# Performance work log

Hardware: AMD Instinct MI355X
Metric: run time of the kernel (lower is better)

## Reference

```python
import jax, jax.numpy as jnp
import numpy as np

EPS = 1e-5
NEG_SLOPE = 0.2

def _bn(x, gamma, beta):
    # BatchNorm1d in training mode: stats over (batch, length) per channel. x: [B,C,N]
    m = jnp.mean(x, axis=(0, 2), keepdims=True)
    v = jnp.mean((x - m) ** 2, axis=(0, 2), keepdims=True)  # biased variance
    return (x - m) * jax.lax.rsqrt(v + EPS) * gamma[None, :, None] + beta[None, :, None]

def setup_inputs() -> dict:
    key = jax.random.key(0)
    ks = jax.random.split(key, 7)
    B, C, N, H = 32, 64, 2048, 128
    s = 1.0 / np.sqrt(C)
    return {
        "x": jax.random.normal(ks[0], (B, C, N), dtype=jnp.float32),
        "wq": jax.random.normal(ks[1], (C, C), dtype=jnp.float32) * s,
        "wk": jax.random.normal(ks[2], (C, C), dtype=jnp.float32) * s,
        "wv": jax.random.normal(ks[3], (C, C), dtype=jnp.float32) * s,
        "w_ff1": jax.random.normal(ks[4], (H, C), dtype=jnp.float32) * s,
        "w_ff2": jax.random.normal(ks[5], (C, H), dtype=jnp.float32) * (1.0 / np.sqrt(H)),
        "bn1_gamma": jnp.ones((C,), dtype=jnp.float32),
        "bn1_beta": jnp.zeros((C,), dtype=jnp.float32),
        "bn2_gamma": jnp.ones((C,), dtype=jnp.float32),
        "bn2_beta": jnp.zeros((C,), dtype=jnp.float32),
    }

def reference(x, wq, wk, wv, w_ff1, w_ff2, bn1_gamma, bn1_beta, bn2_gamma, bn2_beta):
    # x: [B, C, N]; 1x1 convs are per-point channel matmuls
    C = x.shape[1]
    q = jnp.einsum('oc,bcn->bno', wq, x)          # [B,N,C]
    k = jnp.einsum('oc,bcn->bon', wk, x)          # [B,C,N]
    v = jnp.einsum('oc,bcn->bno', wv, x)          # [B,N,C] (v^T)
    energy = jnp.einsum('bnc,bcm->bnm', q, k)     # [B,N,N]
    attention = jax.nn.softmax(energy / jnp.sqrt(jnp.float32(C)), axis=-1)
    x_r = jnp.einsum('bnm,bmc->bcn', attention, v)  # [B,C,N]
    h = _bn(x + x_r, bn1_gamma, bn1_beta)
    ff = jnp.einsum('hc,bcn->bhn', w_ff1, h)      # [B,H,N]
    ff = jnp.where(ff >= 0, ff, NEG_SLOPE * ff)   # LeakyReLU(0.2)
    ff = jnp.einsum('ch,bhn->bcn', w_ff2, ff)     # [B,C,N]
    return _bn(h + ff, bn2_gamma, bn2_beta)
```

## Files before the change

### kernel.cpp

```cpp
#include <hip/hip_runtime.h>

#define B_ 32
#define C_ 64
#define N_ 2048
#define H_ 128
#define MSHIFT 12.0f

typedef unsigned short u16;
typedef unsigned int u32;
typedef float f32x4 __attribute__((ext_vector_type(4)));
typedef float f32x16 __attribute__((ext_vector_type(16)));
typedef __bf16 bf16x8 __attribute__((ext_vector_type(8)));
typedef __bf16 bf16x4 __attribute__((ext_vector_type(4)));
typedef unsigned short u16x4 __attribute__((ext_vector_type(4)));
typedef unsigned int u32x4v __attribute__((ext_vector_type(4)));

#define MFMA(a, b, c) __builtin_amdgcn_mfma_f32_16x16x32_bf16(a, b, c, 0, 0, 0)
#define MFMA32(a, b, c) __builtin_amdgcn_mfma_f32_32x32x16_bf16(a, b, c, 0, 0, 0)
#define EXP2(x) __builtin_amdgcn_exp2f(x)
#define LOG2E 1.44269504088896f

__device__ __forceinline__ int swz(int row, int cb) { return row * 128 + (cb ^ ((row & 7) << 4)); }
__device__ __forceinline__ int swz256(int row, int cb) { return row * 256 + (cb ^ ((row & 7) << 4)); }

__device__ __forceinline__ float b2f(u16 v) {
    union { u32 u; float f; } x; x.u = ((u32)v) << 16; return x.f;
}

__device__ __forceinline__ u32 cvtpk(float lo, float hi) {
    u32 r;
    asm("v_cvt_pk_bf16_f32 %0, %1, %2" : "=v"(r) : "v"(lo), "v"(hi));
    return r;
}

__device__ __forceinline__ bf16x8 pfrag(float p0, float p1, float p2, float p3,
                                        float p4, float p5, float p6, float p7) {
    u32 x1 = cvtpk(p0, p1), x2 = cvtpk(p2, p3);
    u32 y1 = cvtpk(p4, p5), y2 = cvtpk(p6, p7);
    asm volatile("v_permlane32_swap_b32 %0, %1" : "+v"(x1), "+v"(y1));
    asm volatile("v_permlane32_swap_b32 %0, %1" : "+v"(x2), "+v"(y2));
    u32x4v d; d[0] = x1; d[1] = x2; d[2] = y1; d[3] = y2;
    return __builtin_bit_cast(bf16x8, d);
}

__device__ __forceinline__ bf16x8 cvt8(const float* p, float s) {
    f32x4 a = *(const f32x4*)p, b = *(const f32x4*)(p + 4);
    bf16x8 o;
    o[0] = (__bf16)(a[0] * s); o[1] = (__bf16)(a[1] * s);
    o[2] = (__bf16)(a[2] * s); o[3] = (__bf16)(a[3] * s);
    o[4] = (__bf16)(b[0] * s); o[5] = (__bf16)(b[1] * s);
    o[6] = (__bf16)(b[2] * s); o[7] = (__bf16)(b[3] * s);
    return o;
}

__global__ __launch_bounds__(256) void qkv_k(
    const float* __restrict__ x,
    const float* __restrict__ wq, const float* __restrict__ wk, const float* __restrict__ wv,
    const float* __restrict__ w1, const float* __restrict__ w2,
    u16* __restrict__ Qg, u16* __restrict__ Kg, u16* __restrict__ Vg,
    u16* __restrict__ w1b, u16* __restrict__ w2b)
{
    const int b = blockIdx.y, nt = blockIdx.x, t = threadIdx.x;
    const int lane = t & 63, wave = t >> 6, g = lane >> 4, r16 = lane & 15;
    __shared__ __align__(16) u16 xT[128 * 64];
    const int n0 = nt * 128;

    bf16x8 wqf[4][2], wkf[4][2], wvf[4][2];
#pragma unroll
    for (int jt = 0; jt < 4; ++jt)
#pragma unroll
        for (int kc = 0; kc < 2; ++kc) {
            const int ro = (r16 + 16 * jt) * 64 + 8 * g + 32 * kc;
            wqf[jt][kc] = cvt8(wq + ro, 0.125f * LOG2E);
            wkf[jt][kc] = cvt8(wk + ro, 1.0f);
            wvf[jt][kc] = cvt8(wv + ro, 1.0f);
        }

    {
        int c = t >> 5;
        const int nn = (t & 31) * 4;
#pragma unroll
        for (int pass = 0; pass < 8; ++pass, c += 8) {
            f32x4 v = *(const f32x4*)&x[(size_t)(b * 64 + c) * 2048 + n0 + nn];
#pragma unroll
            for (int j = 0; j < 4; ++j)
                xT[swz(nn + j, 2 * c) >> 1] = __builtin_bit_cast(u16, (__bf16)v[j]);
        }
    }
    if (b == 0 && nt == 0) {
        for (int i = t; i < H_ * C_; i += 256) w1b[i] = __builtin_bit_cast(u16, (__bf16)w1[i]);
        for (int i = t; i < C_ * H_; i += 256) w2b[i] = __builtin_bit_cast(u16, (__bf16)w2[i]);
    }
    __syncthreads();

#pragma unroll
    for (int p = 0; p < 2; ++p) {
        const int nt16 = wave * 2 + p;
        bf16x8 xa[2];
#pragma unroll
        for (int kc = 0; kc < 2; ++kc)
            xa[kc] = *(const bf16x8*)&xT[swz(nt16 * 16 + r16, 16 * g + 64 * kc) >> 1];
#pragma unroll
        for (int jt = 0; jt < 4; ++jt) {
            f32x4 aq = {0.f, 0.f, 0.f, 0.f}, ak = {0.f, 0.f, 0.f, 0.f};
            aq = MFMA(wqf[jt][0], xa[0], aq); aq = MFMA(wqf[jt][1], xa[1], aq);
            ak = MFMA(wkf[jt][0], xa[0], ak); ak = MFMA(wkf[jt][1], xa[1], ak);
            bf16x4 qk, kk;
#pragma unroll
            for (int r = 0; r < 4; ++r) { qk[r] = (__bf16)aq[r]; kk[r] = (__bf16)ak[r]; }
            const size_t ro = (size_t)(b * 2048 + n0 + nt16 * 16 + r16) * 64 + 16 * jt + 4 * g;
            *(bf16x4*)&Qg[ro] = qk;
            *(bf16x4*)&Kg[ro] = kk;
        }
#pragma unroll
        for (int it = 0; it < 4; ++it) {
            f32x4 av = {0.f, 0.f, 0.f, 0.f};
            av = MFMA(xa[0], wvf[it][0], av);
            av = MFMA(xa[1], wvf[it][1], av);
            bf16x4 vk;
#pragma unroll
            for (int r = 0; r < 4; ++r) vk[r] = (__bf16)av[r];
            *(bf16x4*)&Vg[(size_t)(b * 64 + 16 * it + r16) * 2048 + n0 + nt16 * 16 + 4 * g] = vk;
        }
    }
}

__global__ __launch_bounds__(256) void attn_k(
    const u16* __restrict__ Qg, const u16* __restrict__ Kg, const u16* __restrict__ Vg,
    const float* __restrict__ x, u16* __restrict__ yb,
    float* __restrict__ ps, float* __restrict__ pq)
{
    const int t = threadIdx.x;
    const int lane = t & 63, wave = t >> 6, q = lane & 31, hi = lane >> 5;
    const int L = blockIdx.x;
    const int xcd = L & 7, slot = L >> 3;
    const int b = xcd * 4 + (slot >> 4);
    const int qt = slot & 15;

    __shared__ __align__(16) u16 Lds16[16384];
    char* lds = (char*)Lds16;

    const int n0 = qt * 128 + wave * 32;
    const int n = n0 + q;

    bf16x8 qf[4];
    {
        const u16* qrow = Qg + (size_t)(b * 2048 + n) * 64 + 8 * hi;
#pragma unroll
        for (int kc = 0; kc < 4; ++kc)
            qf[kc] = *(const bf16x8*)(qrow + 16 * kc);
    }
    bf16x8 ones;
#pragma unroll
    for (int i = 0; i < 8; ++i) ones[i] = (__bf16)1.0f;

    f32x16 acc[2], accl;
#pragma unroll
    for (int r = 0; r < 16; ++r) { acc[0][r] = 0.f; acc[1][r] = 0.f; accl[r] = 0.f; }

    const char* Kgb = (const char*)Kg + (size_t)b * 2048 * 128;
    const char* Vgb = (const char*)Vg + (size_t)b * 64 * 4096;
    const int srcxor = (((lane & 7) ^ (lane >> 3)) << 4);
    const int rowb = wave * 16 + (lane >> 3);

    auto stage = [&](int kvt, int buf) {
#pragma unroll
        for (int j = 0; j < 2; ++j) {
            const char* gk = Kgb + (size_t)(kvt * 64 + rowb + 8 * j) * 128 + srcxor;
            const char* gv = Vgb + (size_t)(rowb + 8 * j) * 4096 + kvt * 128 + srcxor;
            char* lk = lds + buf * 8192 + (wave * 2 + j) * 1024;
            __builtin_amdgcn_global_load_lds(
                (const __attribute__((address_space(1))) void*)gk,
                (__attribute__((address_space(3))) void*)lk, 16, 0, 0);
            __builtin_amdgcn_global_load_lds(
                (const __attribute__((address_space(1))) void*)gv,
                (__attribute__((address_space(3))) void*)(lk + 16384), 16, 0, 0);
        }
    };

    auto tile = [&](int kvt, int buf) {
        __syncthreads();
        if (kvt + 1 < 32) stage(kvt + 1, buf ^ 1);
        const char* Kc = lds + buf * 8192;
        const char* Vc = Kc + 16384;

        f32x16 st[2];
        __builtin_amdgcn_s_setprio(1);
#pragma unroll
        for (int it = 0; it < 2; ++it) {
            f32x16 a;
#pragma unroll
            for (int r = 0; r < 16; ++r) a[r] = -MSHIFT;
#pragma unroll
            for (int kc = 0; kc < 4; ++kc) {
                bf16x8 kf = *(const bf16x8*)(Kc + swz(32 * it + q, 32 * kc + 16 * hi));
                a = MFMA32(kf, qf[kc], a);
            }
            st[it] = a;
        }
        __builtin_amdgcn_s_setprio(0);

        bf16x8 vf[2][4];
#pragma unroll
        for (int ct = 0; ct < 2; ++ct)
#pragma unroll
            for (int mc = 0; mc < 4; ++mc)
                vf[ct][mc] = *(const bf16x8*)(Vc + swz(32 * ct + q, 32 * mc + 16 * hi));

#pragma unroll
        for (int it = 0; it < 2; ++it)
#pragma unroll
            for (int r = 0; r < 16; ++r) st[it][r] = EXP2(st[it][r]);

        bf16x8 pf0 = pfrag(st[0][0], st[0][1], st[0][2], st[0][3],
                           st[0][4], st[0][5], st[0][6], st[0][7]);
        bf16x8 pf1 = pfrag(st[0][8], st[0][9], st[0][10], st[0][11],
                           st[0][12], st[0][13], st[0][14], st[0][15]);
        bf16x8 pf2 = pfrag(st[1][0], st[1][1], st[1][2], st[1][3],
                           st[1][4], st[1][5], st[1][6], st[1][7]);
        bf16x8 pf3 = pfrag(st[1][8], st[1][9], st[1][10], st[1][11],
                           st[1][12], st[1][13], st[1][14], st[1][15]);
        __builtin_amdgcn_s_setprio(1);
#pragma unroll
        for (int ct = 0; ct < 2; ++ct) {
            acc[ct] = MFMA32(vf[ct][0], pf0, acc[ct]);
            acc[ct] = MFMA32(vf[ct][1], pf1, acc[ct]);
            acc[ct] = MFMA32(vf[ct][2], pf2, acc[ct]);
            acc[ct] = MFMA32(vf[ct][3], pf3, acc[ct]);
        }
        accl = MFMA32(ones, pf0, accl);
        accl = MFMA32(ones, pf1, accl);
        accl = MFMA32(ones, pf2, accl);
        accl = MFMA32(ones, pf3, accl);
        __builtin_amdgcn_s_setprio(0);
    };

    stage(0, 0);
#pragma unroll 1
    for (int kvt = 0; kvt < 32; kvt += 2) {
        tile(kvt, 0);
        tile(kvt + 1, 1);
    }

    const float inv = 1.0f / accl[0];
    float sv[2][16], qv[2][16];
#pragma unroll
    for (int ct = 0; ct < 2; ++ct)
#pragma unroll
        for (int r = 0; r < 16; ++r) {
            const int c = 32 * ct + (r & 3) + 8 * (r >> 2) + 4 * hi;
            const float o = acc[ct][r] * inv + x[(size_t)(b * 64 + c) * 2048 + n];
            sv[ct][r] = o;
            qv[ct][r] = o * o;
        }
#pragma unroll
    for (int ct = 0; ct < 2; ++ct)
#pragma unroll
        for (int grp = 0; grp < 4; ++grp) {
            bf16x4 ov;
#pragma unroll
            for (int r = 0; r < 4; ++r) ov[r] = (__bf16)sv[ct][4 * grp + r];
            *(bf16x4*)&yb[(size_t)(b * 2048 + n) * 64 + 32 * ct + 8 * grp + 4 * hi] = ov;
        }
#pragma unroll
    for (int d = 1; d <= 16; d <<= 1)
#pragma unroll
        for (int ct = 0; ct < 2; ++ct)
#pragma unroll
            for (int r = 0; r < 16; ++r) {
                sv[ct][r] += __shfl_xor(sv[ct][r], d, 64);
                qv[ct][r] += __shfl_xor(qv[ct][r], d, 64);
            }
    __syncthreads();
    float* sb = (float*)lds;
    if (q == 0) {
#pragma unroll
        for (int ct = 0; ct < 2; ++ct)
#pragma unroll
            for (int r = 0; r < 16; ++r) {
                const int c = 32 * ct + (r & 3) + 8 * (r >> 2) + 4 * hi;
                sb[wave * 64 + c] = sv[ct][r];
                sb[256 + wave * 64 + c] = qv[ct][r];
            }
    }
    __syncthreads();
    if (t < 64) {
        ps[L * 64 + t] = sb[t] + sb[64 + t] + sb[128 + t] + sb[192 + t];
        pq[L * 64 + t] = sb[256 + t] + sb[320 + t] + sb[384 + t] + sb[448 + t];
    }
}

__global__ __launch_bounds__(256) void finalize_k(
    const float* __restrict__ psum, const float* __restrict__ psq,
    const float* __restrict__ gamma, const float* __restrict__ beta,
    float* __restrict__ ss, int nblk)
{
    const int c = blockIdx.x, t = threadIdx.x;
    const int lane = t & 63, wave = t >> 6;
    float s = 0.f, q = 0.f;
    for (int bl = t; bl < nblk; bl += 256) {
        s += psum[bl * 64 + c];
        q += psq[bl * 64 + c];
    }
#pragma unroll
    for (int d = 1; d <= 32; d <<= 1) {
        s += __shfl_xor(s, d, 64);
        q += __shfl_xor(q, d, 64);
    }
    __shared__ float ls[4], lq[4];
    if (lane == 0) { ls[wave] = s; lq[wave] = q; }
    __syncthreads();
    if (t == 0) {
        s = ls[0] + ls[1] + ls[2] + ls[3];
        q = lq[0] + lq[1] + lq[2] + lq[3];
        const float mean = s * (1.0f / 65536.0f);
        const float var  = q * (1.0f / 65536.0f) - mean * mean;
        const float sc   = rsqrtf(var + 1e-5f) * gamma[c];
        ss[c] = sc;
        ss[64 + c] = beta[c] - mean * sc;
    }
}

__global__ __launch_bounds__(256) void ff_k(
    const u16* __restrict__ y, const float* __restrict__ ss1,
    const u16* __restrict__ w1b, const u16* __restrict__ w2b,
    u16* __restrict__ zb, float* __restrict__ ps, float* __restrict__ pq)
{
    const int b = blockIdx.y, nt = blockIdx.x, t = threadIdx.x;
    const int lane = t & 63, wave = t >> 6, g = lane >> 4, r16 = lane & 15;
    const int L = blockIdx.y * gridDim.x + blockIdx.x;
    __shared__ __align__(16) u16 hT[64 * 64];
    __shared__ __align__(16) float hf[64 * 68];
    __shared__ __align__(16) u16 pb[4][16 * 128];
    __shared__ float sc1[64], sh1[64];
    if (t < 64) { sc1[t] = ss1[t]; sh1[t] = ss1[64 + t]; }
    __syncthreads();
    const int n0 = nt * 64;
    {
        const int i = t >> 2, c0 = (t & 3) * 16;
        u16 yb16[16] __attribute__((aligned(16)));
        *(uint4*)&yb16[0] = *(const uint4*)&y[(size_t)(b * 2048 + n0 + i) * 64 + c0];
        *(uint4*)&yb16[8] = *(const uint4*)&y[(size_t)(b * 2048 + n0 + i) * 64 + c0 + 8];
        u16 hb[16] __attribute__((aligned(16)));
#pragma unroll
        for (int q4 = 0; q4 < 4; ++q4) {
            f32x4 hv;
#pragma unroll
            for (int j = 0; j < 4; ++j) {
                const int c = c0 + 4 * q4 + j;
                hv[j] = b2f(yb16[4 * q4 + j]) * sc1[c] + sh1[c];
                hb[4 * q4 + j] = __builtin_bit_cast(u16, (__bf16)hv[j]);
            }
            *(f32x4*)&hf[i * 68 + c0 + 4 * q4] = hv;
        }
        *(uint4*)&hT[swz(i, 2 * c0) >> 1]      = *(const uint4*)&hb[0];
        *(uint4*)&hT[swz(i, 2 * c0 + 16) >> 1] = *(const uint4*)&hb[8];
    }
    __syncthreads();

    bf16x8 ha[2];
#pragma unroll
    for (int kc = 0; kc < 2; ++kc)
        ha[kc] = *(const bf16x8*)&hT[swz(wave * 16 + r16, 16 * g + 64 * kc) >> 1];
#pragma unroll
    for (int it = 0; it < 8; ++it) {
        f32x4 a = {0.f, 0.f, 0.f, 0.f};
#pragma unroll
        for (int kc = 0; kc < 2; ++kc) {
            bf16x8 w1f = *(const bf16x8*)&w1b[(r16 + 16 * it) * 64 + 8 * g + 32 * kc];
            a = MFMA(w1f, ha[kc], a);
        }
        u16x4 pk;
#pragma unroll
        for (int r = 0; r < 4; ++r) {
            const float rv = a[r] >= 0.f ? a[r] : 0.2f * a[r];
            pk[r] = __builtin_bit_cast(u16, (__bf16)rv);
        }
        *(u16x4*)&pb[wave][swz256(r16, 2 * (16 * it + 4 * g)) >> 1] = pk;
    }
    bf16x8 pa[4];
#pragma unroll
    for (int kc = 0; kc < 4; ++kc)
        pa[kc] = *(const bf16x8*)&pb[wave][swz256(r16, 16 * g + 64 * kc) >> 1];
    const int nl = wave * 16 + r16;
    float sv[4][4], qv[4][4];
#pragma unroll
    for (int jt = 0; jt < 4; ++jt) {
        f32x4 a = {0.f, 0.f, 0.f, 0.f};
#pragma unroll
        for (int kc = 0; kc < 4; ++kc) {
            bf16x8 w2f = *(const bf16x8*)&w2b[(r16 + 16 * jt) * 128 + 8 * g + 32 * kc];
            a = MFMA(w2f, pa[kc], a);
        }
        f32x4 h4 = *(const f32x4*)&hf[nl * 68 + 16 * jt + 4 * g];
        bf16x4 zk;
#pragma unroll
        for (int r = 0; r < 4; ++r) {
            a[r] += h4[r];
            sv[jt][r] = a[r];
            qv[jt][r] = a[r] * a[r];
            zk[r] = (__bf16)a[r];
        }
        *(bf16x4*)&zb[(size_t)(b * 2048 + n0 + nl) * 64 + 16 * jt + 4 * g] = zk;
    }
#pragma unroll
    for (int d = 1; d <= 8; d <<= 1)
#pragma unroll
        for (int jt = 0; jt < 4; ++jt)
#pragma unroll
            for (int r = 0; r < 4; ++r) {
                sv[jt][r] += __shfl_xor(sv[jt][r], d, 64);
                qv[jt][r] += __shfl_xor(qv[jt][r], d, 64);
            }
    __syncthreads();
    float* sb = (float*)&pb[0][0];
    if (r16 == 0) {
#pragma unroll
        for (int jt = 0; jt < 4; ++jt)
#pragma unroll
            for (int r = 0; r < 4; ++r) {
                const int c = 16 * jt + 4 * g + r;
                sb[wave * 64 + c] = sv[jt][r];
                sb[256 + wave * 64 + c] = qv[jt][r];
            }
    }
    __syncthreads();
    if (t < 64) {
        ps[L * 64 + t] = sb[t] + sb[64 + t] + sb[128 + t] + sb[192 + t];
        pq[L * 64 + t] = sb[256 + t] + sb[320 + t] + sb[384 + t] + sb[448 + t];
    }
}

__global__ __launch_bounds__(256) void bnout_k(
    const u16* __restrict__ zb, const float* __restrict__ ss2, float* __restrict__ out)
{
    const int b = blockIdx.y, nt = blockIdx.x, t = threadIdx.x;
    __shared__ float tile[64 * 68];
    __shared__ float sc2[64], sh2[64];
    if (t < 64) { sc2[t] = ss2[t]; sh2[t] = ss2[64 + t]; }
    __syncthreads();
    const int n0 = nt * 64;
    {
        const int i = t >> 2, c0 = (t & 3) * 16;
        u16 zb16[16] __attribute__((aligned(16)));
        *(uint4*)&zb16[0] = *(const uint4*)&zb[(size_t)(b * 2048 + n0 + i) * 64 + c0];
        *(uint4*)&zb16[8] = *(const uint4*)&zb[(size_t)(b * 2048 + n0 + i) * 64 + c0 + 8];
#pragma unroll
        for (int q4 = 0; q4 < 4; ++q4) {
            f32x4 tv;
#pragma unroll
            for (int j = 0; j < 4; ++j) {
                const int c = c0 + 4 * q4 + j;
                tv[j] = b2f(zb16[4 * q4 + j]) * sc2[c] + sh2[c];
            }
            *(f32x4*)&tile[i * 68 + c0 + 4 * q4] = tv;
        }
    }
    __syncthreads();
    {
        const int c = t >> 2, j0 = (t & 3) * 16;
#pragma unroll
        for (int q4 = 0; q4 < 4; ++q4) {
            f32x4 ov;
#pragma unroll
            for (int j = 0; j < 4; ++j)
                ov[j] = tile[(j0 + 4 * q4 + j) * 68 + c];
            *(f32x4*)&out[(size_t)(b * 64 + c) * 2048 + n0 + j0 + 4 * q4] = ov;
        }
    }
}

extern "C" void kernel_launch(void* const* d_in, const int* in_sizes, int n_in,
                              void* d_out, int out_size, void* d_ws, size_t ws_size,
                              hipStream_t stream)
{
    const float* x   = (const float*)d_in[0];
    const float* wq  = (const float*)d_in[1];
    const float* wk  = (const float*)d_in[2];
    const float* wv  = (const float*)d_in[3];
    const float* w1  = (const float*)d_in[4];
    const float* w2  = (const float*)d_in[5];
    const float* g1  = (const float*)d_in[6];
    const float* be1 = (const float*)d_in[7];
    const float* g2  = (const float*)d_in[8];
    const float* be2 = (const float*)d_in[9];
    float* out = (float*)d_out;

    char* w = (char*)d_ws;
    u16* Qg = (u16*)w;   w += (size_t)B_ * N_ * C_ * 2;
    u16* Kg = (u16*)w;   w += (size_t)B_ * N_ * C_ * 2;
    u16* Vg = (u16*)w;   w += (size_t)B_ * N_ * C_ * 2;
    u16* yb = (u16*)w;   w += (size_t)B_ * N_ * C_ * 2;
    u16* zb = (u16*)w;   w += (size_t)B_ * N_ * C_ * 2;
    u16* w1b = (u16*)w;  w += (size_t)H_ * C_ * 2;
    u16* w2b = (u16*)w;  w += (size_t)C_ * H_ * 2;
    float* ps1 = (float*)w; w += 1024 * 64 * 4;
    float* pq1 = (float*)w; w += 1024 * 64 * 4;
    float* ps2 = (float*)w; w += 1024 * 64 * 4;
    float* pq2 = (float*)w; w += 1024 * 64 * 4;
    float* ss1 = (float*)w; w += 128 * 4;
    float* ss2 = (float*)w; w += 128 * 4;

    const dim3 blk(256);
    hipLaunchKernelGGL(qkv_k,   dim3(16, 32), blk, 0, stream, x, wq, wk, wv, w1, w2, Qg, Kg, Vg, w1b, w2b);
    hipLaunchKernelGGL(attn_k,  dim3(512),    blk, 0, stream, Qg, Kg, Vg, x, yb, ps1, pq1);
    hipLaunchKernelGGL(finalize_k, dim3(64),  blk, 0, stream, ps1, pq1, g1, be1, ss1, 512);
    hipLaunchKernelGGL(ff_k,    dim3(32, 32), blk, 0, stream, yb, ss1, w1b, w2b, zb, ps2, pq2);
    hipLaunchKernelGGL(finalize_k, dim3(64),  blk, 0, stream, ps2, pq2, g2, be2, ss2, 1024);
    hipLaunchKernelGGL(bnout_k, dim3(32, 32), blk, 0, stream, zb, ss2, out);
}
```

Baseline: 124.0 us.

## Process two query sub-tiles per wave to reuse K/V fragments in attention

Each wave now handles 64 query rows (two 32-row sub-tiles) instead of 32. K and V fragments loaded from LDS are reused across both sub-tiles, and the grid is halved to 256 blocks. The softmax row sum is now accumulated with VALU adds plus a cross-half shuffle, replacing the extra MFMA against a ones vector. This cuts LDS reads and MFMA work per query, but raises register pressure and halves the block count, which on a 256-CU part may leave some CUs idle.

```diff
diff --git a/kernel.cpp b/kernel.cpp
--- a/kernel.cpp
+++ b/kernel.cpp
@@ -134,29 +134,31 @@
     const int lane = t & 63, wave = t >> 6, q = lane & 31, hi = lane >> 5;
     const int L = blockIdx.x;
     const int xcd = L & 7, slot = L >> 3;
-    const int b = xcd * 4 + (slot >> 4);
-    const int qt = slot & 15;
+    const int b = xcd * 4 + (slot >> 3);
+    const int qt = slot & 7;
 
     __shared__ __align__(16) u16 Lds16[16384];
     char* lds = (char*)Lds16;
 
-    const int n0 = qt * 128 + wave * 32;
-    const int n = n0 + q;
-
-    bf16x8 qf[4];
-    {
-        const u16* qrow = Qg + (size_t)(b * 2048 + n) * 64 + 8 * hi;
+    const int n0 = qt * 256 + wave * 64;
+
+    bf16x8 qf[2][4];
+#pragma unroll
+    for (int u = 0; u < 2; ++u) {
+        const u16* qrow = Qg + (size_t)(b * 2048 + n0 + 32 * u + q) * 64 + 8 * hi;
 #pragma unroll
         for (int kc = 0; kc < 4; ++kc)
-            qf[kc] = *(const bf16x8*)(qrow + 16 * kc);
-    }
-    bf16x8 ones;
-#pragma unroll
-    for (int i = 0; i < 8; ++i) ones[i] = (__bf16)1.0f;
-
-    f32x16 acc[2], accl;
-#pragma unroll
-    for (int r = 0; r < 16; ++r) { acc[0][r] = 0.f; acc[1][r] = 0.f; accl[r] = 0.f; }
+            qf[u][kc] = *(const bf16x8*)(qrow + 16 * kc);
+    }
+
+    f32x16 acc[2][2];
+#pragma unroll
+    for (int u = 0; u < 2; ++u)
+#pragma unroll
+        for (int ct = 0; ct < 2; ++ct)
+#pragma unroll
+            for (int r = 0; r < 16; ++r) acc[u][ct][r] = 0.f;
+    float lp[2] = {0.f, 0.f};
 
     const char* Kgb = (const char*)Kg + (size_t)b * 2048 * 128;
     const char* Vgb = (const char*)Vg + (size_t)b * 64 * 4096;
@@ -184,55 +186,64 @@
         const char* Kc = lds + buf * 8192;
         const char* Vc = Kc + 16384;
 
-        f32x16 st[2];
+        bf16x8 kf[8], vf[8];
+#pragma unroll
+        for (int i = 0; i < 8; ++i)
+            kf[i] = *(const bf16x8*)(Kc + swz(32 * (i >> 2) + q, 32 * (i & 3) + 16 * hi));
+#pragma unroll
+        for (int i = 0; i < 8; ++i)
+            vf[i] = *(const bf16x8*)(Vc + swz(32 * (i >> 2) + q, 32 * (i & 3) + 16 * hi));
+
+        f32x16 st[2][2];
         __builtin_amdgcn_s_setprio(1);
 #pragma unroll
-        for (int it = 0; it < 2; ++it) {
-            f32x16 a;
-#pragma unroll
-            for (int r = 0; r < 16; ++r) a[r] = -MSHIFT;
-#pragma unroll
-            for (int kc = 0; kc < 4; ++kc) {
-                bf16x8 kf = *(const bf16x8*)(Kc + swz(32 * it + q, 32 * kc + 16 * hi));
-                a = MFMA32(kf, qf[kc], a);
-            }
-            st[it] = a;
-        }
+        for (int u = 0; u < 2; ++u)
+#pragma unroll
+            for (int it = 0; it < 2; ++it) {
+                f32x16 a;
+#pragma unroll
+                for (int r = 0; r < 16; ++r) a[r] = -MSHIFT;
+#pragma unroll
+                for (int kc = 0; kc < 4; ++kc)
+                    a = MFMA32(kf[4 * it + kc], qf[u][kc], a);
+                st[u][it] = a;
+            }
         __builtin_amdgcn_s_setprio(0);
 
-        bf16x8 vf[2][4];
-#pragma unroll
-        for (int ct = 0; ct < 2; ++ct)
-#pragma unroll
-            for (int mc = 0; mc < 4; ++mc)
-                vf[ct][mc] = *(const bf16x8*)(Vc + swz(32 * ct + q, 32 * mc + 16 * hi));
-
-#pragma unroll
-        for (int it = 0; it < 2; ++it)
-#pragma unroll
-            for (int r = 0; r < 16; ++r) st[it][r] = EXP2(st[it][r]);
-
-        bf16x8 pf0 = pfrag(st[0][0], st[0][1], st[0][2], st[0][3],
-                           st[0][4], st[0][5], st[0][6], st[0][7]);
-        bf16x8 pf1 = pfrag(st[0][8], st[0][9], st[0][10], st[0][11],
-                           st[0][12], st[0][13], st[0][14], st[0][15]);
-        bf16x8 pf2 = pfrag(st[1][0], st[1][1], st[1][2], st[1][3],
-                           st[1][4], st[1][5], st[1][6], st[1][7]);
-        bf16x8 pf3 = pfrag(st[1][8], st[1][9], st[1][10], st[1][11],
-                           st[1][12], st[1][13], st[1][14], st[1][15]);
-        __builtin_amdgcn_s_setprio(1);
-#pragma unroll
-        for (int ct = 0; ct < 2; ++ct) {
-            acc[ct] = MFMA32(vf[ct][0], pf0, acc[ct]);
-            acc[ct] = MFMA32(vf[ct][1], pf1, acc[ct]);
-            acc[ct] = MFMA32(vf[ct][2], pf2, acc[ct]);
-            acc[ct] = MFMA32(vf[ct][3], pf3, acc[ct]);
-        }
-        accl = MFMA32(ones, pf0, accl);
-        accl = MFMA32(ones, pf1, accl);
-        accl = MFMA32(ones, pf2, accl);
-        accl = MFMA32(ones, pf3, accl);
-        __builtin_amdgcn_s_setprio(0);
+#pragma unroll
+        for (int u = 0; u < 2; ++u) {
+#pragma unroll
+            for (int it = 0; it < 2; ++it)
+#pragma unroll
+                for (int r = 0; r < 16; ++r) st[u][it][r] = EXP2(st[u][it][r]);
+            float ls = 0.f;
+#pragma unroll
+            for (int it = 0; it < 2; ++it) {
+                float a0 = (st[u][it][0] + st[u][it][1]) + (st[u][it][2] + st[u][it][3]);
+                float a1 = (st[u][it][4] + st[u][it][5]) + (st[u][it][6] + st[u][it][7]);
+                float a2 = (st[u][it][8] + st[u][it][9]) + (st[u][it][10] + st[u][it][11]);
+                float a3 = (st[u][it][12] + st[u][it][13]) + (st[u][it][14] + st[u][it][15]);
+                ls += (a0 + a1) + (a2 + a3);
+            }
+            lp[u] += ls;
+            bf16x8 pf0 = pfrag(st[u][0][0], st[u][0][1], st[u][0][2], st[u][0][3],
+                               st[u][0][4], st[u][0][5], st[u][0][6], st[u][0][7]);
+            bf16x8 pf1 = pfrag(st[u][0][8], st[u][0][9], st[u][0][10], st[u][0][11],
+                               st[u][0][12], st[u][0][13], st[u][0][14], st[u][0][15]);
+            bf16x8 pf2 = pfrag(st[u][1][0], st[u][1][1], st[u][1][2], st[u][1][3],
+                               st[u][1][4], st[u][1][5], st[u][1][6], st[u][1][7]);
+            bf16x8 pf3 = pfrag(st[u][1][8], st[u][1][9], st[u][1][10], st[u][1][11],
+                               st[u][1][12], st[u][1][13], st[u][1][14], st[u][1][15]);
+            __builtin_amdgcn_s_setprio(1);
+#pragma unroll
+            for (int ct = 0; ct < 2; ++ct) {
+                acc[u][ct] = MFMA32(vf[4 * ct + 0], pf0, acc[u][ct]);
+                acc[u][ct] = MFMA32(vf[4 * ct + 1], pf1, acc[u][ct]);
+                acc[u][ct] = MFMA32(vf[4 * ct + 2], pf2, acc[u][ct]);
+                acc[u][ct] = MFMA32(vf[4 * ct + 3], pf3, acc[u][ct]);
+            }
+            __builtin_amdgcn_s_setprio(0);
+        }
     };
 
     stage(0, 0);
@@ -242,26 +253,37 @@
         tile(kvt + 1, 1);
     }
 
-    const float inv = 1.0f / accl[0];
+    float inv[2];
+#pragma unroll
+    for (int u = 0; u < 2; ++u) {
+        const float l = lp[u] + __shfl_xor(lp[u], 32, 64);
+        inv[u] = 1.0f / l;
+    }
     float sv[2][16], qv[2][16];
 #pragma unroll
     for (int ct = 0; ct < 2; ++ct)
 #pragma unroll
-        for (int r = 0; r < 16; ++r) {
-            const int c = 32 * ct + (r & 3) + 8 * (r >> 2) + 4 * hi;
-            const float o = acc[ct][r] * inv + x[(size_t)(b * 64 + c) * 2048 + n];
-            sv[ct][r] = o;
-            qv[ct][r] = o * o;
-        }
-#pragma unroll
-    for (int ct = 0; ct < 2; ++ct)
-#pragma unroll
-        for (int grp = 0; grp < 4; ++grp) {
-            bf16x4 ov;
-#pragma unroll
-            for (int r = 0; r < 4; ++r) ov[r] = (__bf16)sv[ct][4 * grp + r];
-            *(bf16x4*)&yb[(size_t)(b * 2048 + n) * 64 + 32 * ct + 8 * grp + 4 * hi] = ov;
-        }
+        for (int r = 0; r < 16; ++r) { sv[ct][r] = 0.f; qv[ct][r] = 0.f; }
+#pragma unroll
+    for (int u = 0; u < 2; ++u) {
+        const int n = n0 + 32 * u + q;
+#pragma unroll
+        for (int ct = 0; ct < 2; ++ct)
+#pragma unroll
+            for (int grp = 0; grp < 4; ++grp) {
+                bf16x4 ov;
+#pragma unroll
+                for (int j = 0; j < 4; ++j) {
+                    const int r = 4 * grp + j;
+                    const int c = 32 * ct + j + 8 * grp + 4 * hi;
+                    const float o = acc[u][ct][r] * inv[u] + x[(size_t)(b * 64 + c) * 2048 + n];
+                    sv[ct][r] += o;
+                    qv[ct][r] += o * o;
+                    ov[j] = (__bf16)o;
+                }
+                *(bf16x4*)&yb[(size_t)(b * 2048 + n) * 64 + 32 * ct + 8 * grp + 4 * hi] = ov;
+            }
+    }
 #pragma unroll
     for (int d = 1; d <= 16; d <<= 1)
 #pragma unroll
@@ -503,8 +525,8 @@
 
     const dim3 blk(256);
     hipLaunchKernelGGL(qkv_k,   dim3(16, 32), blk, 0, stream, x, wq, wk, wv, w1, w2, Qg, Kg, Vg, w1b, w2b);
-    hipLaunchKernelGGL(attn_k,  dim3(512),    blk, 0, stream, Qg, Kg, Vg, x, yb, ps1, pq1);
-    hipLaunchKernelGGL(finalize_k, dim3(64),  blk, 0, stream, ps1, pq1, g1, be1, ss1, 512);
+    hipLaunchKernelGGL(attn_k,  dim3(256),    blk, 0, stream, Qg, Kg, Vg, x, yb, ps1, pq1);
+    hipLaunchKernelGGL(finalize_k, dim3(64),  blk, 0, stream, ps1, pq1, g1, be1, ss1, 256);
     hipLaunchKernelGGL(ff_k,    dim3(32, 32), blk, 0, stream, yb, ss1, w1b, w2b, zb, ps2, pq2);
     hipLaunchKernelGGL(finalize_k, dim3(64),  blk, 0, stream, ps2, pq2, g2, be2, ss2, 1024);
     hipLaunchKernelGGL(bnout_k, dim3(32, 32), blk, 0, stream, zb, ss2, out);
```

Result: slower. 126.8 us (+2.2%).
